# Performance work log

Hardware: AMD Instinct MI355X
Metric: run time of the kernel (lower is better)

## Reference

```python
import jax, jax.numpy as jnp
import numpy as np

D_MODEL = 1024
N_HEADS = 16
DFF = 4096
B, S = 2, 2048
EPS = 1e-6


def _dense_params(key, d_in, d_out):
    kw, kb = jax.random.split(key)
    w = jax.random.normal(kw, (d_in, d_out), jnp.float32) * 0.02
    b = jax.random.normal(kb, (d_out,), jnp.float32) * 0.02
    return w, b


def setup_inputs() -> dict:
    key = jax.random.key(0)
    ks = jax.random.split(key, 20)
    inp = {
        "x": jax.random.normal(ks[0], (B, S, D_MODEL), jnp.float32),
        "enc_output": jax.random.normal(ks[1], (B, S, D_MODEL), jnp.float32),
        # causal look-ahead mask: 1 where attention is NOT allowed
        "look_ahead_mask": jnp.triu(jnp.ones((S, S), jnp.float32), k=1)[None, None],
        "padding_mask": (jax.random.uniform(ks[2], (B, 1, 1, S)) < 0.1).astype(jnp.float32),
    }
    names = ["mha1_wq", "mha1_wk", "mha1_wv", "mha1_wo",
             "mha2_wq", "mha2_wk", "mha2_wv", "mha2_wo"]
    for i, n in enumerate(names):
        w, b = _dense_params(ks[3 + i], D_MODEL, D_MODEL)
        inp[n] = w
        inp[n.replace("w", "b")] = b
    inp["ffn_w1"], inp["ffn_b1"] = _dense_params(ks[11], D_MODEL, DFF)
    inp["ffn_w2"], inp["ffn_b2"] = _dense_params(ks[12], DFF, D_MODEL)
    for i, n in enumerate(["ln1", "ln2", "ln3"]):
        inp[n + "_g"] = jnp.ones((D_MODEL,), jnp.float32)
        inp[n + "_b"] = jnp.zeros((D_MODEL,), jnp.float32)
    return inp


def _layernorm(x, g, b):
    mu = jnp.mean(x, axis=-1, keepdims=True)
    var = jnp.mean(jnp.square(x - mu), axis=-1, keepdims=True)
    return (x - mu) * jax.lax.rsqrt(var + EPS) * g + b


def _mha(v, k, q, mask, wq, bq, wk, bk, wv, bv, wo, bo):
    Bq, Sq, D = q.shape
    depth = D // N_HEADS

    def split(t):  # [B,S,D] -> [B,H,S,depth]
        return t.reshape(t.shape[0], -1, N_HEADS, depth).transpose(0, 2, 1, 3)

    qh = split(q @ wq + bq)
    kh = split(k @ wk + bk)
    vh = split(v @ wv + bv)
    logits = jnp.einsum("bhqd,bhkd->bhqk", qh, kh) / jnp.sqrt(jnp.float32(depth))
    if mask is not None:
        logits = logits + mask * (-1e9)
    attn = jax.nn.softmax(logits, axis=-1)
    out = jnp.einsum("bhqk,bhkd->bhqd", attn, vh)
    out = out.transpose(0, 2, 1, 3).reshape(Bq, Sq, D)
    return out @ wo + bo


def reference(x, enc_output, look_ahead_mask, padding_mask,
              mha1_wq, mha1_bq, mha1_wk, mha1_bk, mha1_wv, mha1_bv, mha1_wo, mha1_bo,
              mha2_wq, mha2_bq, mha2_wk, mha2_bk, mha2_wv, mha2_bv, mha2_wo, mha2_bo,
              ffn_w1, ffn_b1, ffn_w2, ffn_b2,
              ln1_g, ln1_b, ln2_g, ln2_b, ln3_g, ln3_b):
    # self-attention (training=False -> dropout is identity)
    attn1 = _mha(x, x, x, look_ahead_mask,
                 mha1_wq, mha1_bq, mha1_wk, mha1_bk, mha1_wv, mha1_bv, mha1_wo, mha1_bo)
    out1 = _layernorm(x + attn1, ln1_g, ln1_b)
    # cross-attention: q from decoder, k/v from encoder output
    attn2 = _mha(enc_output, enc_output, out1, padding_mask,
                 mha2_wq, mha2_bq, mha2_wk, mha2_bk, mha2_wv, mha2_bv, mha2_wo, mha2_bo)
    out2 = _layernorm(out1 + attn2, ln2_g, ln2_b)
    ffn = jax.nn.relu(out2 @ ffn_w1 + ffn_b1) @ ffn_w2 + ffn_b2
    return _layernorm(out2 + ffn, ln3_g, ln3_b)
```

## Files before the change

kernel.cpp:

```cpp
#include <hip/hip_runtime.h>
#include <hip/hip_bf16.h>
#include <stdint.h>

#define DM   1024
#define NH   16
#define SS   2048
#define BB   2
#define MT   4096

typedef __attribute__((ext_vector_type(8))) short short8;
typedef __attribute__((ext_vector_type(4))) float f32x4;

typedef __attribute__((address_space(1))) const unsigned int as1_uint;
typedef __attribute__((address_space(3))) unsigned int as3_uint;

__device__ __forceinline__ void async16(const void* g, void* l) {
  __builtin_amdgcn_global_load_lds((as1_uint*)g, (as3_uint*)l, 16, 0, 0);
}

#define WAITV(n) asm volatile("s_waitcnt vmcnt(" #n ")" ::: "memory")
#define BARRIER_SB() do { __builtin_amdgcn_s_barrier(); __builtin_amdgcn_sched_barrier(0); } while (0)

__device__ __forceinline__ unsigned short f2bf(float f) {
  union { float f; unsigned u; } c; c.f = f;
  unsigned r = c.u + 0x7fffu + ((c.u >> 16) & 1u);
  return (unsigned short)(r >> 16);
}

__device__ __forceinline__ unsigned cvt_pk_bf16(float lo, float hi) {
  unsigned r;
  asm("v_cvt_pk_bf16_f32 %0, %1, %2" : "=v"(r) : "v"(lo), "v"(hi));
  return r;
}

__global__ __launch_bounds__(256) void k_f32_to_bf16(
    const float* __restrict__ in, unsigned short* __restrict__ out, int n) {
  int i = (blockIdx.x * 256 + threadIdx.x) * 4;
  if (i >= n) return;
  float4 v = *(const float4*)(in + i);
  uint2 u;
  u.x = (unsigned)f2bf(v.x) | ((unsigned)f2bf(v.y) << 16);
  u.y = (unsigned)f2bf(v.z) | ((unsigned)f2bf(v.w) << 16);
  *(uint2*)(out + i) = u;
}

__global__ __launch_bounds__(256) void k_transpose_bf16(
    const float* __restrict__ in, unsigned short* __restrict__ out, int R, int C) {
  __shared__ float t[32][33];
  int c0 = blockIdx.x * 32, r0 = blockIdx.y * 32;
  int tx = threadIdx.x, ty = threadIdx.y;
#pragma unroll
  for (int i = 0; i < 4; i++)
    t[ty + i * 8][tx] = in[(size_t)(r0 + ty + i * 8) * C + c0 + tx];
  __syncthreads();
#pragma unroll
  for (int i = 0; i < 4; i++)
    out[(size_t)(c0 + ty + i * 8) * R + r0 + tx] = f2bf(t[tx][ty + i * 8]);
}

template<int BM, int OUT_MODE, bool RELU, bool RESID, bool SPLITK>
__global__ __launch_bounds__(256) void k_gemm(
    const unsigned short* __restrict__ A,
    const unsigned short* __restrict__ Bt,
    const float* __restrict__ bias,
    const float* __restrict__ resid,
    void* __restrict__ outp, void* __restrict__ outp2,
    int M, int N, int K, int KS) {
  __shared__ unsigned short Alds[3][BM * 32];
  __shared__ unsigned short Blds[3][128 * 32];
  int tid = threadIdx.x;
  int w = tid >> 6, lane = tid & 63;
  int l15 = lane & 15, l4 = lane >> 4;
  int brow = blockIdx.y * BM, bcol = blockIdx.x * 128;

  constexpr int MR = 4;
  constexpr int NR = (BM == 128) ? 4 : 2;
  int wr = (BM == 128) ? (w >> 1) : 0;
  int wc = (BM == 128) ? (w & 1) : w;
  int rbase = wr * 64;
  int cbase = wc * (NR * 16);

  f32x4 acc[MR][NR];
#pragma unroll
  for (int i = 0; i < MR; i++)
#pragma unroll
    for (int j = 0; j < NR; j++) acc[i][j] = (f32x4){0.f, 0.f, 0.f, 0.f};

#define STAGEG(bufi, kk) do {                                                  \
    _Pragma("unroll")                                                          \
    for (int c = 0; c < BM / 64; c++) {                                        \
      int elem = (c * 256 + tid) * 8;                                          \
      int row = elem >> 5, col = elem & 31;                                    \
      async16(A + (size_t)(brow + row) * K + (kk) + col, &Alds[bufi][elem]);   \
    }                                                                          \
    _Pragma("unroll")                                                          \
    for (int c = 0; c < 2; c++) {                                              \
      int elem = (c * 256 + tid) * 8;                                          \
      int row = elem >> 5, col = elem & 31;                                    \
      async16(Bt + (size_t)(bcol + row) * K + (kk) + col, &Blds[bufi][elem]);  \
    } } while (0)

  int kbeg = SPLITK ? blockIdx.z * KS : 0;
  int nk = KS / 32;
  STAGEG(0, kbeg);
  if (nk > 1) {
    STAGEG(1, kbeg + 32);
    if (BM == 128) WAITV(4); else WAITV(3);
  } else {
    WAITV(0);
  }
  BARRIER_SB();

  for (int t = 0; t < nk; t++) {
    int buf = t % 3;
    if (t + 2 < nk) STAGEG((t + 2) % 3, kbeg + (t + 2) * 32);
    short8 af[MR], bfr[NR];
#pragma unroll
    for (int i = 0; i < MR; i++)
      af[i] = *(const short8*)&Alds[buf][(rbase + i * 16 + l15) * 32 + l4 * 8];
#pragma unroll
    for (int j = 0; j < NR; j++)
      bfr[j] = *(const short8*)&Blds[buf][(cbase + j * 16 + l15) * 32 + l4 * 8];
#pragma unroll
    for (int i = 0; i < MR; i++)
#pragma unroll
      for (int j = 0; j < NR; j++)
        acc[i][j] = __builtin_amdgcn_mfma_f32_16x16x32_bf16(af[i], bfr[j], acc[i][j], 0, 0, 0);
    if (t + 2 < nk) {
      if (BM == 128) WAITV(4); else WAITV(3);
    } else if (t + 1 < nk) {
      WAITV(0);
    }
    if (t + 1 < nk) BARRIER_SB();
  }
#undef STAGEG

  void* op = (SPLITK && blockIdx.z) ? outp2 : outp;
#pragma unroll
  for (int i = 0; i < MR; i++)
#pragma unroll
    for (int j = 0; j < NR; j++) {
      int row = brow + rbase + i * 16 + l4 * 4;
      int col = bcol + cbase + j * 16 + l15;
      float bs = (SPLITK || !bias) ? 0.f : bias[col];
#pragma unroll
      for (int r = 0; r < 4; r++) {
        float v = acc[i][j][r] + bs;
        if (RESID) v += resid[(size_t)(row + r) * N + col];
        if (RELU) v = fmaxf(v, 0.f);
        if (OUT_MODE == 0) ((float*)op)[(size_t)(row + r) * N + col] = v;
        else               ((unsigned short*)op)[(size_t)(row + r) * N + col] = f2bf(v);
      }
    }
}

__global__ __launch_bounds__(256) void k_gemm_qkv(
    const unsigned short* __restrict__ a0, const unsigned short* __restrict__ a1,
    const unsigned short* __restrict__ a2,
    const unsigned short* __restrict__ Bt,
    const float* __restrict__ b0, const float* __restrict__ b1, const float* __restrict__ b2,
    unsigned short* __restrict__ o0, unsigned short* __restrict__ o1, unsigned short* __restrict__ o2,
    int vmat, int M, int K) {
  __shared__ unsigned short Alds[3][128 * 32];
  __shared__ unsigned short Blds[3][128 * 32];
  int tid = threadIdx.x;
  int w = tid >> 6, lane = tid & 63;
  int wr = w >> 1, wc = w & 1;
  int l15 = lane & 15, l4 = lane >> 4;
  int z = blockIdx.z;
  const unsigned short* A  = (z == 0) ? a0 : (z == 1) ? a1 : a2;
  const unsigned short* Bz = Bt + (size_t)z * 1048576;
  int brow = blockIdx.y * 128, bcol = blockIdx.x * 128;

  f32x4 acc[4][4];
#pragma unroll
  for (int i = 0; i < 4; i++)
#pragma unroll
    for (int j = 0; j < 4; j++) acc[i][j] = (f32x4){0.f, 0.f, 0.f, 0.f};

#define STAGEQ(bufi, kk) do {                                                  \
    _Pragma("unroll")                                                          \
    for (int c = 0; c < 2; c++) {                                              \
      int elem = (c * 256 + tid) * 8;                                          \
      int row = elem >> 5, col = elem & 31;                                    \
      async16(A + (size_t)(brow + row) * K + (kk) + col, &Alds[bufi][elem]);   \
      async16(Bz + (size_t)(bcol + row) * K + (kk) + col, &Blds[bufi][elem]);  \
    } } while (0)

  int nk = K / 32;
  STAGEQ(0, 0);
  STAGEQ(1, 32);
  WAITV(4);
  BARRIER_SB();

  for (int t = 0; t < nk; t++) {
    int buf = t % 3;
    if (t + 2 < nk) STAGEQ((t + 2) % 3, (t + 2) * 32);
    short8 af[4], bfr[4];
#pragma unroll
    for (int i = 0; i < 4; i++) {
      af[i]  = *(const short8*)&Alds[buf][(wr * 64 + i * 16 + l15) * 32 + l4 * 8];
      bfr[i] = *(const short8*)&Blds[buf][(wc * 64 + i * 16 + l15) * 32 + l4 * 8];
    }
#pragma unroll
    for (int i = 0; i < 4; i++)
#pragma unroll
      for (int j = 0; j < 4; j++)
        acc[i][j] = __builtin_amdgcn_mfma_f32_16x16x32_bf16(af[i], bfr[j], acc[i][j], 0, 0, 0);
    if (t + 2 < nk) WAITV(4);
    else if (t + 1 < nk) WAITV(0);
    if (t + 1 < nk) BARRIER_SB();
  }
#undef STAGEQ

  const float* bias = (z == 0) ? b0 : (z == 1) ? b1 : b2;
  unsigned short* op = (z == 0) ? o0 : (z == 1) ? o1 : o2;
  bool tr = (z == vmat);
#pragma unroll
  for (int i = 0; i < 4; i++)
#pragma unroll
    for (int j = 0; j < 4; j++) {
      int row = brow + wr * 64 + i * 16 + l4 * 4;
      int colL = bcol + wc * 64 + j * 16 + l15;
      float bs = bias[colL];
#pragma unroll
      for (int r = 0; r < 4; r++) {
        float v = acc[i][j][r] + bs;
        if (tr) op[(size_t)colL * M + row + r] = f2bf(v);
        else    op[(size_t)(row + r) * 1024 + colL] = f2bf(v);
      }
    }
}

template<bool CAUSAL>
__global__ __launch_bounds__(256) void k_attn(
    const unsigned short* __restrict__ Q,
    const unsigned short* __restrict__ Kb,
    const unsigned short* __restrict__ Vt,
    const float* __restrict__ pm,
    unsigned short* __restrict__ out) {
  __shared__ unsigned short Klds[3][64 * 64];
  __shared__ unsigned short Vlds[3][64 * 64];
  __shared__ unsigned short Pw[4][2][16 * 72];
  int tid = threadIdx.x, w = tid >> 6, lane = tid & 63;
  int l15 = lane & 15, l4 = lane >> 4;
  int qt = CAUSAL ? ((int)gridDim.x - 1 - (int)blockIdx.x) : blockIdx.x;
  int h = blockIdx.y, b = blockIdx.z;
  int qbase = qt * 128 + w * 32;
  const float SC = 0.125f * 1.44269504089f;

  short8 qf[2][2];
#pragma unroll
  for (int f = 0; f < 2; f++) {
    size_t qrow = (size_t)b * SS + qbase + f * 16 + l15;
#pragma unroll
    for (int ks = 0; ks < 2; ks++)
      qf[f][ks] = *(const short8*)(Q + qrow * DM + h * 64 + ks * 32 + l4 * 8);
  }

  float mrow[2] = {-1e30f, -1e30f}, lrow[2] = {0.f, 0.f};
  f32x4 accO[2][4];
#pragma unroll
  for (int f = 0; f < 2; f++)
#pragma unroll
    for (int d = 0; d < 4; d++) accO[f][d] = (f32x4){0.f, 0.f, 0.f, 0.f};

#define STAGE(bufi, kt_) do {                                                  \
    _Pragma("unroll")                                                          \
    for (int c = 0; c < 2; c++) {                                              \
      int e0 = w * 1024 + c * 512;                                             \
      int elem = e0 + lane * 8;                                                \
      int row_ = elem >> 6;                                                    \
      int col_ = (elem & 63) ^ ((row_ & 7) << 3);                              \
      async16(Kb + (size_t)(b * SS + (kt_) * 64 + row_) * DM + h * 64 + col_,  \
              &Klds[bufi][elem]);                                              \
      async16(Vt + (size_t)(h * 64 + row_) * MT + b * SS + (kt_) * 64 + col_,  \
              &Vlds[bufi][elem]);                                              \
    } } while (0)

  int ktend = CAUSAL ? (2 * qt + 1) : (SS / 64 - 1);
  STAGE(0, 0);
  if (ktend >= 1) { STAGE(1, 1); WAITV(4); } else { WAITV(0); }
  BARRIER_SB();

  for (int kt = 0; kt <= ktend; kt++) {
    int buf = kt % 3;
    if (kt + 2 <= ktend) STAGE((kt + 2) % 3, kt + 2);

    bool active = !CAUSAL || (kt * 64 <= qbase + 31);
    if (active) {
      f32x4 sa[2][4];
#pragma unroll
      for (int f = 0; f < 2; f++)
#pragma unroll
        for (int nt = 0; nt < 4; nt++) sa[f][nt] = (f32x4){0.f, 0.f, 0.f, 0.f};
      __builtin_amdgcn_s_setprio(1);
#pragma unroll
      for (int ks = 0; ks < 2; ks++)
#pragma unroll
        for (int nt = 0; nt < 4; nt++) {
          int kr = nt * 16 + l15;
          short8 kf = *(const short8*)&Klds[buf][kr * 64 + ((ks * 32 + l4 * 8) ^ ((kr & 7) << 3))];
#pragma unroll
          for (int f = 0; f < 2; f++)
            sa[f][nt] = __builtin_amdgcn_mfma_f32_16x16x32_bf16(kf, qf[f][ks], sa[f][nt], 0, 0, 0);
        }
      __builtin_amdgcn_s_setprio(0);

      float pmb[16];
      if (!CAUSAL) {
#pragma unroll
        for (int nt = 0; nt < 4; nt++) {
          float4 pmv = *(const float4*)(pm + b * SS + kt * 64 + nt * 16 + l4 * 4);
#pragma unroll
          for (int r = 0; r < 4; r++) pmb[nt * 4 + r] = ((const float*)&pmv)[r] * -1e30f;
        }
      }
      bool diag = CAUSAL && (kt * 64 + 63 > qbase);

#pragma unroll
      for (int f = 0; f < 2; f++) {
        float sv[16], tmax = -3e38f;
        if (CAUSAL && !diag) {
#pragma unroll
          for (int i = 0; i < 16; i++) {
            float s = sa[f][i >> 2][i & 3] * SC;
            sv[i] = s; tmax = fmaxf(tmax, s);
          }
        } else if (CAUSAL) {
#pragma unroll
          for (int nt = 0; nt < 4; nt++)
#pragma unroll
            for (int r = 0; r < 4; r++) {
              float s = sa[f][nt][r] * SC;
              int kg = kt * 64 + nt * 16 + l4 * 4 + r;
              int qg = qbase + f * 16 + l15;
              if (kg > qg) s = -1e30f;
              sv[nt * 4 + r] = s; tmax = fmaxf(tmax, s);
            }
        } else {
#pragma unroll
          for (int i = 0; i < 16; i++) {
            float s = fmaf(sa[f][i >> 2][i & 3], SC, pmb[i]);
            sv[i] = s; tmax = fmaxf(tmax, s);
          }
        }
        tmax = fmaxf(tmax, __shfl_xor(tmax, 16));
        tmax = fmaxf(tmax, __shfl_xor(tmax, 32));

        if (!__all(tmax - mrow[f] <= 8.f)) {
          float mnew = fmaxf(mrow[f], tmax);
          float corr = exp2f(mrow[f] - mnew);
          mrow[f] = mnew;
          lrow[f] *= corr;
#pragma unroll
          for (int r = 0; r < 4; r++) {
            float cq = __shfl(corr, l4 * 4 + r);
#pragma unroll
            for (int dt = 0; dt < 4; dt++) accO[f][dt][r] *= cq;
          }
        }

        float p[16], psum = 0.f;
#pragma unroll
        for (int i = 0; i < 16; i++) { p[i] = exp2f(sv[i] - mrow[f]); psum += p[i]; }
        psum += __shfl_xor(psum, 16);
        psum += __shfl_xor(psum, 32);
        lrow[f] += psum;

#pragma unroll
        for (int nt = 0; nt < 4; nt++) {
          uint2 u;
          u.x = cvt_pk_bf16(p[nt * 4 + 0], p[nt * 4 + 1]);
          u.y = cvt_pk_bf16(p[nt * 4 + 2], p[nt * 4 + 3]);
          *(uint2*)&Pw[w][f][l15 * 72 + nt * 16 + l4 * 4] = u;
        }
      }

      __builtin_amdgcn_s_setprio(1);
#pragma unroll
      for (int ks = 0; ks < 2; ks++) {
        short8 pf0 = *(const short8*)&Pw[w][0][l15 * 72 + ks * 32 + l4 * 8];
        short8 pf1 = *(const short8*)&Pw[w][1][l15 * 72 + ks * 32 + l4 * 8];
#pragma unroll
        for (int dt = 0; dt < 4; dt++) {
          int vr = dt * 16 + l15;
          short8 vf = *(const short8*)&Vlds[buf][vr * 64 + ((ks * 32 + l4 * 8) ^ ((vr & 7) << 3))];
          accO[0][dt] = __builtin_amdgcn_mfma_f32_16x16x32_bf16(pf0, vf, accO[0][dt], 0, 0, 0);
          accO[1][dt] = __builtin_amdgcn_mfma_f32_16x16x32_bf16(pf1, vf, accO[1][dt], 0, 0, 0);
        }
      }
      __builtin_amdgcn_s_setprio(0);
    }

    if (kt + 2 <= ktend) WAITV(4);
    else if (kt + 1 <= ktend) WAITV(0);
    if (kt + 1 <= ktend) BARRIER_SB();
  }
#undef STAGE

#pragma unroll
  for (int f = 0; f < 2; f++)
#pragma unroll
    for (int r = 0; r < 4; r++) {
      float lq = __shfl(lrow[f], l4 * 4 + r);
      float inv = 1.f / lq;
      size_t row = (size_t)b * SS + qbase + f * 16 + l4 * 4 + r;
#pragma unroll
      for (int dt = 0; dt < 4; dt++)
        out[row * DM + h * 64 + dt * 16 + l15] = f2bf(accO[f][dt][r] * inv);
    }
}

__global__ __launch_bounds__(256) void k_ln(
    const float* __restrict__ in, const float* __restrict__ in2,
    const float* __restrict__ resid, const float* __restrict__ bias,
    const float* __restrict__ g, const float* __restrict__ bb,
    float* __restrict__ outf, unsigned short* __restrict__ outb) {
  int row = blockIdx.x, tid = threadIdx.x;
  int w = tid >> 6;
  __shared__ float red[4];
  float4 v = *(const float4*)(in + (size_t)row * 1024 + tid * 4);
  if (in2) {
    float4 v2 = *(const float4*)(in2 + (size_t)row * 1024 + tid * 4);
    v.x += v2.x; v.y += v2.y; v.z += v2.z; v.w += v2.w;
  }
  if (resid) {
    float4 v2 = *(const float4*)(resid + (size_t)row * 1024 + tid * 4);
    v.x += v2.x; v.y += v2.y; v.z += v2.z; v.w += v2.w;
  }
  if (bias) {
    float4 v2 = *(const float4*)(bias + tid * 4);
    v.x += v2.x; v.y += v2.y; v.z += v2.z; v.w += v2.w;
  }
  float s = v.x + v.y + v.z + v.w;
#pragma unroll
  for (int d = 1; d < 64; d <<= 1) s += __shfl_xor(s, d);
  if ((tid & 63) == 0) red[w] = s;
  __syncthreads();
  float mu = (red[0] + red[1] + red[2] + red[3]) * (1.f / 1024.f);
  float d0 = v.x - mu, d1 = v.y - mu, d2 = v.z - mu, d3 = v.w - mu;
  float q = d0 * d0 + d1 * d1 + d2 * d2 + d3 * d3;
#pragma unroll
  for (int d = 1; d < 64; d <<= 1) q += __shfl_xor(q, d);
  __syncthreads();
  if ((tid & 63) == 0) red[w] = q;
  __syncthreads();
  float var = (red[0] + red[1] + red[2] + red[3]) * (1.f / 1024.f);
  float rs = rsqrtf(var + 1e-6f);
  float4 gg = *(const float4*)(g + tid * 4);
  float4 bv = *(const float4*)(bb + tid * 4);
  float y0 = d0 * rs * gg.x + bv.x;
  float y1 = d1 * rs * gg.y + bv.y;
  float y2 = d2 * rs * gg.z + bv.z;
  float y3 = d3 * rs * gg.w + bv.w;
  if (outf) {
    float4 o; o.x = y0; o.y = y1; o.z = y2; o.w = y3;
    *(float4*)(outf + (size_t)row * 1024 + tid * 4) = o;
  }
  if (outb) {
    uint2 u;
    u.x = (unsigned)f2bf(y0) | ((unsigned)f2bf(y1) << 16);
    u.y = (unsigned)f2bf(y2) | ((unsigned)f2bf(y3) << 16);
    *(uint2*)(outb + (size_t)row * 1024 + tid * 4) = u;
  }
}

extern "C" void kernel_launch(void* const* d_in, const int* in_sizes, int n_in,
                              void* d_out, int out_size, void* d_ws, size_t ws_size,
                              hipStream_t stream) {
  const float* x    = (const float*)d_in[0];
  const float* enc  = (const float*)d_in[1];
  const float* pm   = (const float*)d_in[3];
  const float* wq1  = (const float*)d_in[4];   const float* bq1 = (const float*)d_in[5];
  const float* wk1  = (const float*)d_in[6];   const float* bk1 = (const float*)d_in[7];
  const float* wv1  = (const float*)d_in[8];   const float* bv1 = (const float*)d_in[9];
  const float* wo1  = (const float*)d_in[10];  const float* bo1 = (const float*)d_in[11];
  const float* wq2  = (const float*)d_in[12];  const float* bq2 = (const float*)d_in[13];
  const float* wk2  = (const float*)d_in[14];  const float* bk2 = (const float*)d_in[15];
  const float* wv2  = (const float*)d_in[16];  const float* bv2 = (const float*)d_in[17];
  const float* wo2  = (const float*)d_in[18];  const float* bo2 = (const float*)d_in[19];
  const float* fw1  = (const float*)d_in[20];  const float* fb1 = (const float*)d_in[21];
  const float* fw2  = (const float*)d_in[22];  const float* fb2 = (const float*)d_in[23];
  const float* ln1g = (const float*)d_in[24];  const float* ln1b = (const float*)d_in[25];
  const float* ln2g = (const float*)d_in[26];  const float* ln2b = (const float*)d_in[27];
  const float* ln3g = (const float*)d_in[28];  const float* ln3b = (const float*)d_in[29];

  char* ws = (char*)d_ws;
  unsigned short* XB = (unsigned short*)(ws + 0);
  unsigned short* EB = (unsigned short*)(ws + 8388608);
  unsigned short* Qb = (unsigned short*)(ws + 16777216);
  unsigned short* Kb = (unsigned short*)(ws + 25165824);
  unsigned short* Vt = (unsigned short*)(ws + 33554432);
  unsigned short* AT = (unsigned short*)(ws + 41943040);
  float*          T  = (float*)(ws + 50331648);
  float*          R  = (float*)(ws + 67108864);
  unsigned short* RB = (unsigned short*)(ws + 83886080);
  unsigned short* WT0 = (unsigned short*)(ws + 92274688);
  unsigned short* W1T = (unsigned short*)(ws + 92274688 + 16777216);
  unsigned short* W2T = (unsigned short*)(ws + 92274688 + 25165824);
  unsigned short* H   = (unsigned short*)(ws + 0);
  float*          T1  = (float*)(ws + 33554432);
  float*          T1o = (float*)(ws + 16777216);

  k_f32_to_bf16<<<4096, 256, 0, stream>>>(x, XB, MT * DM);
  k_f32_to_bf16<<<4096, 256, 0, stream>>>(enc, EB, MT * DM);
  dim3 tb(32, 8);
  const float* wlist[8] = {wq1, wk1, wv1, wo1, wq2, wk2, wv2, wo2};
  for (int i = 0; i < 8; i++)
    k_transpose_bf16<<<dim3(32, 32), tb, 0, stream>>>(wlist[i], WT0 + (size_t)i * 1048576, 1024, 1024);
  k_transpose_bf16<<<dim3(128, 32), tb, 0, stream>>>(fw1, W1T, 1024, 4096);
  k_transpose_bf16<<<dim3(32, 128), tb, 0, stream>>>(fw2, W2T, 4096, 1024);

  dim3 ga(16, 16, 2);

  k_gemm_qkv<<<dim3(8, 32, 3), 256, 0, stream>>>(XB, XB, XB, WT0, bq1, bk1, bv1,
                                                 Qb, Kb, Vt, 2, MT, DM);
  k_attn<true><<<ga, 256, 0, stream>>>(Qb, Kb, Vt, nullptr, AT);
  k_gemm<64, 0, false, false, true><<<dim3(8, 64, 2), 256, 0, stream>>>(
      AT, WT0 + 3 * 1048576, nullptr, nullptr, T, T1o, MT, DM, DM, 512);
  k_ln<<<4096, 256, 0, stream>>>(T, T1o, x, bo1, ln1g, ln1b, R, RB);

  k_gemm_qkv<<<dim3(8, 32, 3), 256, 0, stream>>>(RB, EB, EB, WT0 + 4 * 1048576,
                                                 bq2, bk2, bv2, Qb, Kb, Vt, 2, MT, DM);
  k_attn<false><<<ga, 256, 0, stream>>>(Qb, Kb, Vt, pm, AT);
  k_gemm<64, 0, false, false, true><<<dim3(8, 64, 2), 256, 0, stream>>>(
      AT, WT0 + 7 * 1048576, nullptr, nullptr, T, T1o, MT, DM, DM, 512);
  k_ln<<<4096, 256, 0, stream>>>(T, T1o, R, bo2, ln2g, ln2b, R, RB);

  k_gemm<128, 1, true, false, false><<<dim3(32, 32), 256, 0, stream>>>(
      RB, W1T, fb1, nullptr, H, nullptr, MT, 4096, DM, 1024);
  k_gemm<64, 0, false, false, true><<<dim3(8, 64, 2), 256, 0, stream>>>(
      H, W2T, nullptr, nullptr, T, T1, MT, DM, 4096, 2048);
  k_ln<<<4096, 256, 0, stream>>>(T, T1, R, fb2, ln3g, ln3b, (float*)d_out, nullptr);
}
```

Measured before the change: 507.4 us.

## Pair causal query tiles per block and defer softmax row-sum reduction

The causal attention kernel now launches half as many blocks, and each block processes two query tiles (qt = 15-x and qt = x) in sequence. This balances the triangular workload so every block does the same amount of work. The per-iteration cross-lane row-sum reduction is dropped; partial sums stay per lane and are reduced once at the end. Row-max reductions for both fragments are interleaved, using ds_swizzle in place of one shuffle. The price is less block-level parallelism in the causal pass (256 blocks on the device) and an extra barrier between passes.

```diff
diff --git a/kernel.cpp b/kernel.cpp
--- a/kernel.cpp
+++ b/kernel.cpp
@@ -31,6 +31,10 @@
   unsigned r;
   asm("v_cvt_pk_bf16_f32 %0, %1, %2" : "=v"(r) : "v"(lo), "v"(hi));
   return r;
+}
+
+__device__ __forceinline__ float swz16(float x) {
+  return __uint_as_float((unsigned)__builtin_amdgcn_ds_swizzle((int)__float_as_uint(x), 0x401F));
 }
 
 __global__ __launch_bounds__(256) void k_f32_to_bf16(
@@ -244,26 +248,9 @@
   __shared__ unsigned short Pw[4][2][16 * 72];
   int tid = threadIdx.x, w = tid >> 6, lane = tid & 63;
   int l15 = lane & 15, l4 = lane >> 4;
-  int qt = CAUSAL ? ((int)gridDim.x - 1 - (int)blockIdx.x) : blockIdx.x;
   int h = blockIdx.y, b = blockIdx.z;
-  int qbase = qt * 128 + w * 32;
   const float SC = 0.125f * 1.44269504089f;
-
-  short8 qf[2][2];
-#pragma unroll
-  for (int f = 0; f < 2; f++) {
-    size_t qrow = (size_t)b * SS + qbase + f * 16 + l15;
-#pragma unroll
-    for (int ks = 0; ks < 2; ks++)
-      qf[f][ks] = *(const short8*)(Q + qrow * DM + h * 64 + ks * 32 + l4 * 8);
-  }
-
-  float mrow[2] = {-1e30f, -1e30f}, lrow[2] = {0.f, 0.f};
-  f32x4 accO[2][4];
-#pragma unroll
-  for (int f = 0; f < 2; f++)
-#pragma unroll
-    for (int d = 0; d < 4; d++) accO[f][d] = (f32x4){0.f, 0.f, 0.f, 0.f};
+  const int NPASS = CAUSAL ? 2 : 1;
 
 #define STAGE(bufi, kt_) do {                                                  \
     _Pragma("unroll")                                                          \
@@ -278,138 +265,176 @@
               &Vlds[bufi][elem]);                                              \
     } } while (0)
 
-  int ktend = CAUSAL ? (2 * qt + 1) : (SS / 64 - 1);
-  STAGE(0, 0);
-  if (ktend >= 1) { STAGE(1, 1); WAITV(4); } else { WAITV(0); }
-  BARRIER_SB();
-
-  for (int kt = 0; kt <= ktend; kt++) {
-    int buf = kt % 3;
-    if (kt + 2 <= ktend) STAGE((kt + 2) % 3, kt + 2);
-
-    bool active = !CAUSAL || (kt * 64 <= qbase + 31);
-    if (active) {
-      f32x4 sa[2][4];
-#pragma unroll
-      for (int f = 0; f < 2; f++)
-#pragma unroll
-        for (int nt = 0; nt < 4; nt++) sa[f][nt] = (f32x4){0.f, 0.f, 0.f, 0.f};
-      __builtin_amdgcn_s_setprio(1);
+  for (int pass = 0; pass < NPASS; pass++) {
+    int qt = CAUSAL ? (pass == 0 ? (15 - (int)blockIdx.x) : (int)blockIdx.x)
+                    : (int)blockIdx.x;
+    int qbase = qt * 128 + w * 32;
+
+    short8 qf[2][2];
+#pragma unroll
+    for (int f = 0; f < 2; f++) {
+      size_t qrow = (size_t)b * SS + qbase + f * 16 + l15;
 #pragma unroll
       for (int ks = 0; ks < 2; ks++)
-#pragma unroll
-        for (int nt = 0; nt < 4; nt++) {
-          int kr = nt * 16 + l15;
-          short8 kf = *(const short8*)&Klds[buf][kr * 64 + ((ks * 32 + l4 * 8) ^ ((kr & 7) << 3))];
-#pragma unroll
-          for (int f = 0; f < 2; f++)
-            sa[f][nt] = __builtin_amdgcn_mfma_f32_16x16x32_bf16(kf, qf[f][ks], sa[f][nt], 0, 0, 0);
-        }
-      __builtin_amdgcn_s_setprio(0);
-
-      float pmb[16];
-      if (!CAUSAL) {
-#pragma unroll
-        for (int nt = 0; nt < 4; nt++) {
-          float4 pmv = *(const float4*)(pm + b * SS + kt * 64 + nt * 16 + l4 * 4);
-#pragma unroll
-          for (int r = 0; r < 4; r++) pmb[nt * 4 + r] = ((const float*)&pmv)[r] * -1e30f;
-        }
-      }
-      bool diag = CAUSAL && (kt * 64 + 63 > qbase);
-
-#pragma unroll
-      for (int f = 0; f < 2; f++) {
-        float sv[16], tmax = -3e38f;
-        if (CAUSAL && !diag) {
-#pragma unroll
-          for (int i = 0; i < 16; i++) {
-            float s = sa[f][i >> 2][i & 3] * SC;
-            sv[i] = s; tmax = fmaxf(tmax, s);
+        qf[f][ks] = *(const short8*)(Q + qrow * DM + h * 64 + ks * 32 + l4 * 8);
+    }
+
+    float mrow[2] = {-1e30f, -1e30f}, lrow[2] = {0.f, 0.f};
+    f32x4 accO[2][4];
+#pragma unroll
+    for (int f = 0; f < 2; f++)
+#pragma unroll
+      for (int d = 0; d < 4; d++) accO[f][d] = (f32x4){0.f, 0.f, 0.f, 0.f};
+
+    int ktend = CAUSAL ? (2 * qt + 1) : (SS / 64 - 1);
+    if (pass) BARRIER_SB();
+    STAGE(0, 0);
+    if (ktend >= 1) { STAGE(1, 1); WAITV(4); } else { WAITV(0); }
+    BARRIER_SB();
+
+    for (int kt = 0; kt <= ktend; kt++) {
+      int buf = kt % 3;
+      if (kt + 2 <= ktend) STAGE((kt + 2) % 3, kt + 2);
+
+      bool active = !CAUSAL || (kt * 64 <= qbase + 31);
+      if (active) {
+        f32x4 sa[2][4];
+#pragma unroll
+        for (int f = 0; f < 2; f++)
+#pragma unroll
+          for (int nt = 0; nt < 4; nt++) sa[f][nt] = (f32x4){0.f, 0.f, 0.f, 0.f};
+        __builtin_amdgcn_s_setprio(1);
+#pragma unroll
+        for (int ks = 0; ks < 2; ks++)
+#pragma unroll
+          for (int nt = 0; nt < 4; nt++) {
+            int kr = nt * 16 + l15;
+            short8 kf = *(const short8*)&Klds[buf][kr * 64 + ((ks * 32 + l4 * 8) ^ ((kr & 7) << 3))];
+#pragma unroll
+            for (int f = 0; f < 2; f++)
+              sa[f][nt] = __builtin_amdgcn_mfma_f32_16x16x32_bf16(kf, qf[f][ks], sa[f][nt], 0, 0, 0);
           }
-        } else if (CAUSAL) {
-#pragma unroll
-          for (int nt = 0; nt < 4; nt++)
-#pragma unroll
-            for (int r = 0; r < 4; r++) {
-              float s = sa[f][nt][r] * SC;
-              int kg = kt * 64 + nt * 16 + l4 * 4 + r;
-              int qg = qbase + f * 16 + l15;
-              if (kg > qg) s = -1e30f;
-              sv[nt * 4 + r] = s; tmax = fmaxf(tmax, s);
-            }
-        } else {
-#pragma unroll
-          for (int i = 0; i < 16; i++) {
-            float s = fmaf(sa[f][i >> 2][i & 3], SC, pmb[i]);
-            sv[i] = s; tmax = fmaxf(tmax, s);
+        __builtin_amdgcn_s_setprio(0);
+
+        float pmb[16];
+        if (!CAUSAL) {
+#pragma unroll
+          for (int nt = 0; nt < 4; nt++) {
+            float4 pmv = *(const float4*)(pm + b * SS + kt * 64 + nt * 16 + l4 * 4);
+#pragma unroll
+            for (int r = 0; r < 4; r++) pmb[nt * 4 + r] = ((const float*)&pmv)[r] * -1e30f;
           }
         }
-        tmax = fmaxf(tmax, __shfl_xor(tmax, 16));
-        tmax = fmaxf(tmax, __shfl_xor(tmax, 32));
-
-        if (!__all(tmax - mrow[f] <= 8.f)) {
-          float mnew = fmaxf(mrow[f], tmax);
-          float corr = exp2f(mrow[f] - mnew);
-          mrow[f] = mnew;
-          lrow[f] *= corr;
-#pragma unroll
-          for (int r = 0; r < 4; r++) {
-            float cq = __shfl(corr, l4 * 4 + r);
-#pragma unroll
-            for (int dt = 0; dt < 4; dt++) accO[f][dt][r] *= cq;
+        bool diag = CAUSAL && (kt * 64 + 63 > qbase);
+
+        float sv[2][16], tm[2];
+#pragma unroll
+        for (int f = 0; f < 2; f++) {
+          float tmax = -3e38f;
+          if (CAUSAL && !diag) {
+#pragma unroll
+            for (int i = 0; i < 16; i++) {
+              float s = sa[f][i >> 2][i & 3] * SC;
+              sv[f][i] = s; tmax = fmaxf(tmax, s);
+            }
+          } else if (CAUSAL) {
+#pragma unroll
+            for (int nt = 0; nt < 4; nt++)
+#pragma unroll
+              for (int r = 0; r < 4; r++) {
+                float s = sa[f][nt][r] * SC;
+                int kg = kt * 64 + nt * 16 + l4 * 4 + r;
+                int qg = qbase + f * 16 + l15;
+                if (kg > qg) s = -1e30f;
+                sv[f][nt * 4 + r] = s; tmax = fmaxf(tmax, s);
+              }
+          } else {
+#pragma unroll
+            for (int i = 0; i < 16; i++) {
+              float s = fmaf(sa[f][i >> 2][i & 3], SC, pmb[i]);
+              sv[f][i] = s; tmax = fmaxf(tmax, s);
+            }
+          }
+          tm[f] = tmax;
+        }
+
+        float sA = swz16(tm[0]);
+        float sB = swz16(tm[1]);
+        tm[0] = fmaxf(tm[0], sA);
+        tm[1] = fmaxf(tm[1], sB);
+        float xA = __shfl_xor(tm[0], 32);
+        float xB = __shfl_xor(tm[1], 32);
+        tm[0] = fmaxf(tm[0], xA);
+        tm[1] = fmaxf(tm[1], xB);
+
+#pragma unroll
+        for (int f = 0; f < 2; f++) {
+          if (!__all(tm[f] - mrow[f] <= 8.f)) {
+            float mnew = fmaxf(mrow[f], tm[f]);
+            float corr = exp2f(mrow[f] - mnew);
+            mrow[f] = mnew;
+            lrow[f] *= corr;
+#pragma unroll
+            for (int r = 0; r < 4; r++) {
+              float cq = __shfl(corr, l4 * 4 + r);
+#pragma unroll
+              for (int dt = 0; dt < 4; dt++) accO[f][dt][r] *= cq;
+            }
+          }
+
+          float p[16], psum = 0.f;
+#pragma unroll
+          for (int i = 0; i < 16; i++) { p[i] = exp2f(sv[f][i] - mrow[f]); psum += p[i]; }
+          lrow[f] += psum;
+
+#pragma unroll
+          for (int nt = 0; nt < 4; nt++) {
+            uint2 u;
+            u.x = cvt_pk_bf16(p[nt * 4 + 0], p[nt * 4 + 1]);
+            u.y = cvt_pk_bf16(p[nt * 4 + 2], p[nt * 4 + 3]);
+            *(uint2*)&Pw[w][f][l15 * 72 + nt * 16 + l4 * 4] = u;
           }
         }
 
-        float p[16], psum = 0.f;
-#pragma unroll
-        for (int i = 0; i < 16; i++) { p[i] = exp2f(sv[i] - mrow[f]); psum += p[i]; }
-        psum += __shfl_xor(psum, 16);
-        psum += __shfl_xor(psum, 32);
-        lrow[f] += psum;
-
-#pragma unroll
-        for (int nt = 0; nt < 4; nt++) {
-          uint2 u;
-          u.x = cvt_pk_bf16(p[nt * 4 + 0], p[nt * 4 + 1]);
-          u.y = cvt_pk_bf16(p[nt * 4 + 2], p[nt * 4 + 3]);
-          *(uint2*)&Pw[w][f][l15 * 72 + nt * 16 + l4 * 4] = u;
+        __builtin_amdgcn_s_setprio(1);
+#pragma unroll
+        for (int ks = 0; ks < 2; ks++) {
+          short8 pf0 = *(const short8*)&Pw[w][0][l15 * 72 + ks * 32 + l4 * 8];
+          short8 pf1 = *(const short8*)&Pw[w][1][l15 * 72 + ks * 32 + l4 * 8];
+#pragma unroll
+          for (int dt = 0; dt < 4; dt++) {
+            int vr = dt * 16 + l15;
+            short8 vf = *(const short8*)&Vlds[buf][vr * 64 + ((ks * 32 + l4 * 8) ^ ((vr & 7) << 3))];
+            accO[0][dt] = __builtin_amdgcn_mfma_f32_16x16x32_bf16(pf0, vf, accO[0][dt], 0, 0, 0);
+            accO[1][dt] = __builtin_amdgcn_mfma_f32_16x16x32_bf16(pf1, vf, accO[1][dt], 0, 0, 0);
+          }
         }
+        __builtin_amdgcn_s_setprio(0);
       }
 
-      __builtin_amdgcn_s_setprio(1);
-#pragma unroll
-      for (int ks = 0; ks < 2; ks++) {
-        short8 pf0 = *(const short8*)&Pw[w][0][l15 * 72 + ks * 32 + l4 * 8];
-        short8 pf1 = *(const short8*)&Pw[w][1][l15 * 72 + ks * 32 + l4 * 8];
-#pragma unroll
-        for (int dt = 0; dt < 4; dt++) {
-          int vr = dt * 16 + l15;
-          short8 vf = *(const short8*)&Vlds[buf][vr * 64 + ((ks * 32 + l4 * 8) ^ ((vr & 7) << 3))];
-          accO[0][dt] = __builtin_amdgcn_mfma_f32_16x16x32_bf16(pf0, vf, accO[0][dt], 0, 0, 0);
-          accO[1][dt] = __builtin_amdgcn_mfma_f32_16x16x32_bf16(pf1, vf, accO[1][dt], 0, 0, 0);
-        }
+      if (kt + 2 <= ktend) WAITV(4);
+      else if (kt + 1 <= ktend) WAITV(0);
+      if (kt + 1 <= ktend) BARRIER_SB();
+    }
+
+#pragma unroll
+    for (int f = 0; f < 2; f++) {
+      lrow[f] += swz16(lrow[f]);
+      lrow[f] += __shfl_xor(lrow[f], 32);
+    }
+#pragma unroll
+    for (int f = 0; f < 2; f++)
+#pragma unroll
+      for (int r = 0; r < 4; r++) {
+        float lq = __shfl(lrow[f], l4 * 4 + r);
+        float inv = 1.f / lq;
+        size_t row = (size_t)b * SS + qbase + f * 16 + l4 * 4 + r;
+#pragma unroll
+        for (int dt = 0; dt < 4; dt++)
+          out[row * DM + h * 64 + dt * 16 + l15] = f2bf(accO[f][dt][r] * inv);
       }
-      __builtin_amdgcn_s_setprio(0);
-    }
-
-    if (kt + 2 <= ktend) WAITV(4);
-    else if (kt + 1 <= ktend) WAITV(0);
-    if (kt + 1 <= ktend) BARRIER_SB();
   }
 #undef STAGE
-
-#pragma unroll
-  for (int f = 0; f < 2; f++)
-#pragma unroll
-    for (int r = 0; r < 4; r++) {
-      float lq = __shfl(lrow[f], l4 * 4 + r);
-      float inv = 1.f / lq;
-      size_t row = (size_t)b * SS + qbase + f * 16 + l4 * 4 + r;
-#pragma unroll
-      for (int dt = 0; dt < 4; dt++)
-        out[row * DM + h * 64 + dt * 16 + l15] = f2bf(accO[f][dt][r] * inv);
-    }
 }
 
 __global__ __launch_bounds__(256) void k_ln(
@@ -512,18 +537,16 @@
   k_transpose_bf16<<<dim3(128, 32), tb, 0, stream>>>(fw1, W1T, 1024, 4096);
   k_transpose_bf16<<<dim3(32, 128), tb, 0, stream>>>(fw2, W2T, 4096, 1024);
 
-  dim3 ga(16, 16, 2);
-
   k_gemm_qkv<<<dim3(8, 32, 3), 256, 0, stream>>>(XB, XB, XB, WT0, bq1, bk1, bv1,
                                                  Qb, Kb, Vt, 2, MT, DM);
-  k_attn<true><<<ga, 256, 0, stream>>>(Qb, Kb, Vt, nullptr, AT);
+  k_attn<true><<<dim3(8, 16, 2), 256, 0, stream>>>(Qb, Kb, Vt, nullptr, AT);
   k_gemm<64, 0, false, false, true><<<dim3(8, 64, 2), 256, 0, stream>>>(
       AT, WT0 + 3 * 1048576, nullptr, nullptr, T, T1o, MT, DM, DM, 512);
   k_ln<<<4096, 256, 0, stream>>>(T, T1o, x, bo1, ln1g, ln1b, R, RB);
 
   k_gemm_qkv<<<dim3(8, 32, 3), 256, 0, stream>>>(RB, EB, EB, WT0 + 4 * 1048576,
                                                  bq2, bk2, bv2, Qb, Kb, Vt, 2, MT, DM);
-  k_attn<false><<<ga, 256, 0, stream>>>(Qb, Kb, Vt, pm, AT);
+  k_attn<false><<<dim3(16, 16, 2), 256, 0, stream>>>(Qb, Kb, Vt, pm, AT);
   k_gemm<64, 0, false, false, true><<<dim3(8, 64, 2), 256, 0, stream>>>(
       AT, WT0 + 7 * 1048576, nullptr, nullptr, T, T1o, MT, DM, DM, 512);
   k_ln<<<4096, 256, 0, stream>>>(T, T1o, R, bo2, ln2g, ln2b, R, RB);
```

Measured after the change: 482.4 us. 1.05x faster.
